# Performance work log

Measured on AMD Instinct MI355X. Metric: run time of the kernel, lower is better.

The kernel has to match this reference:

```python
import jax, jax.numpy as jnp
import numpy as np

NUM_AGENTS = 1000
N_ACTIONS = 16
HIDDEN = 256
COMM_STEPS = 4
B, M = 1024, 64


def setup_inputs() -> dict:
    key = jax.random.key(0)
    ks = jax.random.split(key, 8)
    agent_ids = jax.random.randint(ks[0], (B, M), 0, NUM_AGENTS)
    emb = jax.random.normal(ks[1], (NUM_AGENTS, HIDDEN), dtype=jnp.float32) * 0.1
    s1 = 1.0 / np.sqrt(3 * HIDDEN)
    W1 = jax.random.uniform(ks[2], (3 * HIDDEN, HIDDEN), jnp.float32, -s1, s1)
    b1 = jax.random.uniform(ks[3], (HIDDEN,), jnp.float32, -s1, s1)
    s2 = 1.0 / np.sqrt(HIDDEN)
    W2 = jax.random.uniform(ks[4], (HIDDEN, HIDDEN), jnp.float32, -s2, s2)
    b2 = jax.random.uniform(ks[5], (HIDDEN,), jnp.float32, -s2, s2)
    Wd = jax.random.uniform(ks[6], (HIDDEN, N_ACTIONS), jnp.float32, -s2, s2)
    bd = jax.random.uniform(ks[7], (N_ACTIONS,), jnp.float32, -s2, s2)
    return {"agent_ids": agent_ids, "emb": emb, "W1": W1, "b1": b1,
            "W2": W2, "b2": b2, "Wd": Wd, "bd": bd}


def reference(agent_ids, emb, W1, b1, W2, b2, Wd, bd):
    # h0: (B, M, H) embedding lookup
    h0 = emb[agent_ids]
    h = h0
    m = agent_ids.shape[1]
    inv = 1.0 / (m - 1)
    for _ in range(COMM_STEPS):
        # mean of other agents' hidden states: c_j = (sum_k h_k - h_j)/(M-1)
        c = (jnp.sum(h, axis=1, keepdims=True) - h) * inv
        x = jnp.concatenate([h, c, h0], axis=-1)  # (B, M, 3H)
        delta = jax.nn.relu(jnp.einsum('bmi,ih->bmh', x, W1) + b1)
        delta = jnp.einsum('bmi,ih->bmh', delta, W2) + b2
        h = h + delta  # residual (use_skip=True)
    logits = jnp.einsum('bmh,ha->bma', h, Wd) + bd
    return logits
```

## Files before the change

kernel.cpp:

```cpp
#include <hip/hip_runtime.h>

#define HID 256
#define NB 1024
#define NACT 16

typedef __bf16 bf16x8 __attribute__((ext_vector_type(8)));
typedef float  f32x4  __attribute__((ext_vector_type(4)));

#define HA_LO   32768
#define BUF0    65536
#define BUF1    98304
#define LDS_TOT 131072

#define PREP_N (4 * 65536 + 4096)

__device__ __forceinline__ void gload_lds16(const void* g, void* l) {
    __builtin_amdgcn_global_load_lds(
        (const __attribute__((address_space(1))) void*)g,
        (__attribute__((address_space(3))) void*)l, 16, 0, 0);
}
__device__ __forceinline__ unsigned short f2bf(float x) {
    union { float f; unsigned u; } v; v.f = x;
    unsigned r = v.u + 0x7fff + ((v.u >> 16) & 1);
    return (unsigned short)(r >> 16);
}
__device__ __forceinline__ float bf2f(unsigned short b) {
    union { float f; unsigned u; } v; v.u = ((unsigned)b) << 16;
    return v.f;
}
__device__ __forceinline__ float b2f_lo(unsigned v) { return bf2f((unsigned short)(v & 0xffffu)); }
__device__ __forceinline__ float b2f_hi(unsigned v) { return bf2f((unsigned short)(v >> 16)); }

__global__ __launch_bounds__(256) void prep_k(const float* __restrict__ W1,
                                              const float* __restrict__ W2,
                                              const float* __restrict__ Wd,
                                              unsigned short* __restrict__ WAh, unsigned short* __restrict__ WAl,
                                              unsigned short* __restrict__ WHh, unsigned short* __restrict__ WHl,
                                              unsigned short* __restrict__ WBh, unsigned short* __restrict__ WBl,
                                              unsigned short* __restrict__ WDh, unsigned short* __restrict__ WDl,
                                              float* __restrict__ Wc) {
    int i = blockIdx.x * 256 + threadIdx.x;
    const float inv = 1.0f / 63.0f;
    if (i < 65536) {
        int n = i >> 8, k = i & 255;
        float val = W1[k * 256 + n] - inv * W1[(256 + k) * 256 + n];
        unsigned short hi = f2bf(val);
        WAh[i] = hi; WAl[i] = f2bf(val - bf2f(hi));
    } else if (i < 2 * 65536) {
        int j = i - 65536, n = j >> 8, k = j & 255;
        float val = W1[(512 + k) * 256 + n];
        unsigned short hi = f2bf(val);
        WHh[j] = hi; WHl[j] = f2bf(val - bf2f(hi));
    } else if (i < 3 * 65536) {
        int j = i - 2 * 65536, n = j >> 8, k = j & 255;
        float val = W2[k * 256 + n];
        unsigned short hi = f2bf(val);
        WBh[j] = hi; WBl[j] = f2bf(val - bf2f(hi));
    } else if (i < 4 * 65536) {
        int j = i - 3 * 65536, k = j >> 8, n = j & 255;
        Wc[j] = inv * W1[(256 + k) * 256 + n];
    } else if (i < PREP_N) {
        int j = i - 4 * 65536, a = j >> 8, k = j & 255;
        float val = Wd[k * 16 + a];
        unsigned short hi = f2bf(val);
        WDh[j] = hi; WDl[j] = f2bf(val - bf2f(hi));
    }
}

__device__ __forceinline__ void kloopKar(const unsigned short* __restrict__ Wh,
                                         const unsigned short* __restrict__ Wl,
                                         char* lds, f32x4 (&acc)[2][4],
                                         int tid, int wm, int wn, int l15, int g)
{
    char* hA = lds;
    const int rxA = (l15 & 7) << 4;
    const int rowA0 = (wm * 32 + l15) * 512;
    const int rowA1 = rowA0 + 16 * 512;

    __syncthreads();
    #pragma unroll
    for (int p = 0; p < 2; ++p) {
        int c = p * 512 + tid;
        int n = c >> 2, s = c & 3;
        int sp = s ^ ((n >> 1) & 3);
        gload_lds16(Wh + (size_t)n * 256 + sp * 8, lds + BUF0 + c * 16);
        gload_lds16(Wl + (size_t)n * 256 + sp * 8, lds + BUF0 + 16384 + c * 16);
    }
    __syncthreads();

    #pragma unroll 2
    for (int kq = 0; kq < 8; ++kq) {
        const int cur = kq & 1;
        if (kq + 1 < 8) {
            const int kk = (kq + 1) * 32;
            char* dst = lds + (cur ? BUF0 : BUF1);
            #pragma unroll
            for (int p = 0; p < 2; ++p) {
                int c = p * 512 + tid;
                int n = c >> 2, s = c & 3;
                int sp = s ^ ((n >> 1) & 3);
                gload_lds16(Wh + (size_t)n * 256 + kk + sp * 8, dst + c * 16);
                gload_lds16(Wl + (size_t)n * 256 + kk + sp * 8, dst + 16384 + c * 16);
            }
        }
        const char* bb = lds + (cur ? BUF1 : BUF0);
        const int cb = (kq * 64 + g * 16) ^ rxA;
        bf16x8 a0h = *(const bf16x8*)(hA + rowA0 + cb);
        bf16x8 a1h = *(const bf16x8*)(hA + rowA1 + cb);
        bf16x8 a0l = *(const bf16x8*)(hA + HA_LO + rowA0 + cb);
        bf16x8 a1l = *(const bf16x8*)(hA + HA_LO + rowA1 + cb);
        #pragma unroll
        for (int nt = 0; nt < 4; ++nt) {
            int nn = wn * 64 + nt * 16 + l15;
            int off = nn * 64 + ((g ^ ((nn >> 1) & 3)) << 4);
            bf16x8 bh = *(const bf16x8*)(bb + off);
            bf16x8 bl = *(const bf16x8*)(bb + 16384 + off);
            acc[0][nt] = __builtin_amdgcn_mfma_f32_16x16x32_bf16(a0h, bh, acc[0][nt], 0, 0, 0);
            acc[1][nt] = __builtin_amdgcn_mfma_f32_16x16x32_bf16(a1h, bh, acc[1][nt], 0, 0, 0);
            acc[0][nt] = __builtin_amdgcn_mfma_f32_16x16x32_bf16(a0l, bh, acc[0][nt], 0, 0, 0);
            acc[1][nt] = __builtin_amdgcn_mfma_f32_16x16x32_bf16(a1l, bh, acc[1][nt], 0, 0, 0);
            acc[0][nt] = __builtin_amdgcn_mfma_f32_16x16x32_bf16(a0h, bl, acc[0][nt], 0, 0, 0);
            acc[1][nt] = __builtin_amdgcn_mfma_f32_16x16x32_bf16(a1h, bl, acc[1][nt], 0, 0, 0);
        }
        __syncthreads();
    }
}

__device__ __forceinline__ void STfun(char* lds, const float* __restrict__ Wc, int tid)
{
    char* hA = lds;
    float* Sp = (float*)(lds + BUF0);
    float* Sf = (float*)(lds + BUF0 + 4096);
    float* Tp = (float*)(lds + BUF0 + 8192);
    __syncthreads();
    {
        int ww = tid & 127, gq = tid >> 7;
        float s0 = 0.f, s1 = 0.f;
        #pragma unroll 4
        for (int m = gq * 16; m < gq * 16 + 16; ++m) {
            int byte = m * 512 + ((ww * 4) ^ ((m & 7) << 4));
            unsigned vh = *(const unsigned*)(hA + byte);
            unsigned vl = *(const unsigned*)(hA + HA_LO + byte);
            s0 += b2f_lo(vh) + b2f_lo(vl);
            s1 += b2f_hi(vh) + b2f_hi(vl);
        }
        Sp[gq * 256 + ww * 2] = s0;
        Sp[gq * 256 + ww * 2 + 1] = s1;
    }
    __syncthreads();
    if (tid < 256) Sf[tid] = (Sp[tid] + Sp[256 + tid]) + (Sp[512 + tid] + Sp[768 + tid]);
    __syncthreads();
    {
        int n = tid & 255, kh = tid >> 8;
        float a = 0.f;
        #pragma unroll 8
        for (int k = kh * 128; k < kh * 128 + 128; ++k)
            a += Sf[k] * Wc[(k << 8) + n];
        Tp[kh * 256 + n] = a;
    }
    __syncthreads();
}

__global__ __launch_bounds__(512, 2) void fused_all(
    const int* __restrict__ ids, const float* __restrict__ emb,
    const unsigned short* __restrict__ WAh, const unsigned short* __restrict__ WAl,
    const unsigned short* __restrict__ WHh, const unsigned short* __restrict__ WHl,
    const unsigned short* __restrict__ WBh, const unsigned short* __restrict__ WBl,
    const unsigned short* __restrict__ WDh, const unsigned short* __restrict__ WDl,
    const float* __restrict__ Wc,
    const float* __restrict__ b1, const float* __restrict__ b2,
    const float* __restrict__ bd, float* __restrict__ out)
{
    __shared__ __align__(16) char lds[LDS_TOT];
    const int tid = threadIdx.x;
    const int lane = tid & 63;
    const int w = tid >> 6;
    const int wm = w >> 2, wn = w & 3;
    const int l15 = lane & 15, g = lane >> 4;
    const size_t rowbase = (size_t)blockIdx.x * 64;
    char* hA = lds;
    float* Tp = (float*)(lds + BUF0 + 8192);

    {
        int r = tid >> 3, c0 = (tid & 7) * 32;
        int rx = (r & 7) << 4;
        const float4* src = (const float4*)(emb + (size_t)ids[rowbase + r] * HID + c0);
        char* dh = hA + r * 512;
        #pragma unroll
        for (int j = 0; j < 8; ++j) {
            float4 v = src[j];
            unsigned short h0 = f2bf(v.x), h1 = f2bf(v.y), h2 = f2bf(v.z), h3 = f2bf(v.w);
            unsigned short q0 = f2bf(v.x - bf2f(h0)), q1 = f2bf(v.y - bf2f(h1)),
                           q2 = f2bf(v.z - bf2f(h2)), q3 = f2bf(v.w - bf2f(h3));
            int byte = ((c0 + j * 4) * 2) ^ rx;
            *(uint2*)(dh + byte) = make_uint2((unsigned)h0 | ((unsigned)h1 << 16),
                                             (unsigned)h2 | ((unsigned)h3 << 16));
            *(uint2*)(dh + HA_LO + byte) = make_uint2((unsigned)q0 | ((unsigned)q1 << 16),
                                                      (unsigned)q2 | ((unsigned)q3 << 16));
        }
    }

    float b2r[4];
    #pragma unroll
    for (int nt = 0; nt < 4; ++nt) b2r[nt] = b2[wn * 64 + nt * 16 + l15];

    STfun(lds, Wc, tid);
    float tvr[4];
    #pragma unroll
    for (int nt = 0; nt < 4; ++nt) {
        int col = wn * 64 + nt * 16 + l15;
        tvr[nt] = Tp[col] + Tp[256 + col];
    }

    f32x4 acc[2][4], u0r[2][4];
    #pragma unroll
    for (int mt = 0; mt < 2; ++mt)
        #pragma unroll
        for (int nt = 0; nt < 4; ++nt) acc[mt][nt] = (f32x4){0.f, 0.f, 0.f, 0.f};

    for (int s = 0; s < 4; ++s) {
        if (s == 0) {
            kloopKar(WHh, WHl, lds, acc, tid, wm, wn, l15, g);
            #pragma unroll
            for (int nt = 0; nt < 4; ++nt) {
                float bb = b1[wn * 64 + nt * 16 + l15];
                #pragma unroll
                for (int mt = 0; mt < 2; ++mt)
                    #pragma unroll
                    for (int q = 0; q < 4; ++q) {
                        u0r[mt][nt][q] = acc[mt][nt][q] + bb;
                        acc[mt][nt][q] = 0.f;
                    }
            }
        }
        #pragma unroll
        for (int mt = 0; mt < 2; ++mt)
            #pragma unroll
            for (int nt = 0; nt < 4; ++nt)
                #pragma unroll
                for (int q = 0; q < 4; ++q)
                    acc[mt][nt][q] = tvr[nt] + u0r[mt][nt][q];
        kloopKar(WAh, WAl, lds, acc, tid, wm, wn, l15, g);

        #pragma unroll
        for (int mt = 0; mt < 2; ++mt)
            #pragma unroll
            for (int nt = 0; nt < 4; ++nt)
                #pragma unroll
                for (int q = 0; q < 4; ++q) {
                    int row = wm * 32 + mt * 16 + g * 4 + q;
                    int col = wn * 64 + nt * 16 + l15;
                    int byte = row * 512 + ((col * 2) ^ ((row & 7) << 4));
                    float hres = bf2f(*(const unsigned short*)(hA + byte))
                               + bf2f(*(const unsigned short*)(hA + HA_LO + byte));
                    float a = fmaxf(acc[mt][nt][q], 0.f);
                    unsigned short hi = f2bf(a);
                    *(unsigned short*)(hA + byte) = hi;
                    *(unsigned short*)(hA + HA_LO + byte) = f2bf(a - bf2f(hi));
                    acc[mt][nt][q] = hres + b2r[nt];
                }

        kloopKar(WBh, WBl, lds, acc, tid, wm, wn, l15, g);

        #pragma unroll
        for (int mt = 0; mt < 2; ++mt)
            #pragma unroll
            for (int nt = 0; nt < 4; ++nt)
                #pragma unroll
                for (int q = 0; q < 4; ++q) {
                    int row = wm * 32 + mt * 16 + g * 4 + q;
                    int col = wn * 64 + nt * 16 + l15;
                    int byte = row * 512 + ((col * 2) ^ ((row & 7) << 4));
                    float hv = acc[mt][nt][q];
                    unsigned short hi = f2bf(hv);
                    *(unsigned short*)(hA + byte) = hi;
                    *(unsigned short*)(hA + HA_LO + byte) = f2bf(hv - bf2f(hi));
                    acc[mt][nt][q] = 0.f;
                }

        if (s < 3) {
            STfun(lds, Wc, tid);
            #pragma unroll
            for (int nt = 0; nt < 4; ++nt) {
                int col = wn * 64 + nt * 16 + l15;
                tvr[nt] = Tp[col] + Tp[256 + col];
            }
        }
    }

    __syncthreads();
    {
        float* Dp = (float*)(lds + BUF0);
        f32x4 dacc[4];
        #pragma unroll
        for (int mi = 0; mi < 4; ++mi) dacc[mi] = (f32x4){0.f, 0.f, 0.f, 0.f};
        const int k = w * 32;
        bf16x8 wdh = *(const bf16x8*)(WDh + (size_t)l15 * 256 + k + g * 8);
        bf16x8 wdl = *(const bf16x8*)(WDl + (size_t)l15 * 256 + k + g * 8);
        #pragma unroll
        for (int mi = 0; mi < 4; ++mi) {
            int m = mi * 16 + l15;
            int byte = m * 512 + ((k * 2 + g * 16) ^ ((m & 7) << 4));
            bf16x8 hh = *(const bf16x8*)(hA + byte);
            bf16x8 hl = *(const bf16x8*)(hA + HA_LO + byte);
            dacc[mi] = __builtin_amdgcn_mfma_f32_16x16x32_bf16(wdh, hh, dacc[mi], 0, 0, 0);
            dacc[mi] = __builtin_amdgcn_mfma_f32_16x16x32_bf16(wdl, hh, dacc[mi], 0, 0, 0);
            dacc[mi] = __builtin_amdgcn_mfma_f32_16x16x32_bf16(wdh, hl, dacc[mi], 0, 0, 0);
        }
        #pragma unroll
        for (int mi = 0; mi < 4; ++mi)
            #pragma unroll
            for (int q = 0; q < 4; ++q)
                Dp[w * 1024 + (mi * 16 + l15) * 16 + g * 4 + q] = dacc[mi][q];
    }
    __syncthreads();
    {
        float* Dp = (float*)(lds + BUF0);
        int m = tid >> 3, a0 = (tid & 7) * 2;
        float o0 = bd[a0], o1 = bd[a0 + 1];
        #pragma unroll
        for (int w8 = 0; w8 < 8; ++w8) {
            o0 += Dp[w8 * 1024 + m * 16 + a0];
            o1 += Dp[w8 * 1024 + m * 16 + a0 + 1];
        }
        *(float2*)(out + ((size_t)rowbase + m) * NACT + a0) = make_float2(o0, o1);
    }
}

extern "C" void kernel_launch(void* const* d_in, const int* in_sizes, int n_in,
                              void* d_out, int out_size, void* d_ws, size_t ws_size,
                              hipStream_t stream) {
    const int*   ids = (const int*)d_in[0];
    const float* emb = (const float*)d_in[1];
    const float* W1  = (const float*)d_in[2];
    const float* b1  = (const float*)d_in[3];
    const float* W2  = (const float*)d_in[4];
    const float* b2  = (const float*)d_in[5];
    const float* Wd  = (const float*)d_in[6];
    const float* bd  = (const float*)d_in[7];
    float* out = (float*)d_out;

    char* p = (char*)d_ws;
    unsigned short* WAh = (unsigned short*)p; p += 65536 * 2;
    unsigned short* WAl = (unsigned short*)p; p += 65536 * 2;
    unsigned short* WHh = (unsigned short*)p; p += 65536 * 2;
    unsigned short* WHl = (unsigned short*)p; p += 65536 * 2;
    unsigned short* WBh = (unsigned short*)p; p += 65536 * 2;
    unsigned short* WBl = (unsigned short*)p; p += 65536 * 2;
    unsigned short* WDh = (unsigned short*)p; p += 4096 * 2;
    unsigned short* WDl = (unsigned short*)p; p += 4096 * 2;
    float* Wc = (float*)p;

    prep_k<<<(PREP_N + 255) / 256, 256, 0, stream>>>(W1, W2, Wd, WAh, WAl, WHh, WHl,
                                                     WBh, WBl, WDh, WDl, Wc);
    fused_all<<<NB, 512, 0, stream>>>(ids, emb, WAh, WAl, WHh, WHl, WBh, WBl,
                                      WDh, WDl, Wc, b1, b2, bd, out);
}
```

Measured before the change: 327.7 us.

## Stream weight fragments directly from global/L2 instead of staging through LDS

The prep kernel now writes the split bf16 weights pre-swizzled into MFMA fragment order. The GEMM loop loads B fragments directly from global memory (expected to hit L2) rather than double-buffering them into LDS. Each wave now covers all 64 rows by 32 columns instead of a 32x64 tile, and the per-k-step block barriers are gone. LDS use per block drops from 128KB to 80KB. In exchange, every wave loads its weights from L2 with nothing in between to hide the latency, and the final logits reduction uses only 4 waves.

```diff
diff --git a/kernel.cpp b/kernel.cpp
--- a/kernel.cpp
+++ b/kernel.cpp
@@ -8,17 +8,11 @@
 typedef float  f32x4  __attribute__((ext_vector_type(4)));
 
 #define HA_LO   32768
-#define BUF0    65536
-#define BUF1    98304
-#define LDS_TOT 131072
+#define OV      65536
+#define LDS_TOT 81920
 
 #define PREP_N (4 * 65536 + 4096)
 
-__device__ __forceinline__ void gload_lds16(const void* g, void* l) {
-    __builtin_amdgcn_global_load_lds(
-        (const __attribute__((address_space(1))) void*)g,
-        (__attribute__((address_space(3))) void*)l, 16, 0, 0);
-}
 __device__ __forceinline__ unsigned short f2bf(float x) {
     union { float f; unsigned u; } v; v.f = x;
     unsigned r = v.u + 0x7fff + ((v.u >> 16) & 1);
@@ -41,21 +35,22 @@
                                               float* __restrict__ Wc) {
     int i = blockIdx.x * 256 + threadIdx.x;
     const float inv = 1.0f / 63.0f;
-    if (i < 65536) {
-        int n = i >> 8, k = i & 255;
-        float val = W1[k * 256 + n] - inv * W1[(256 + k) * 256 + n];
+    if (i < 3 * 65536) {
+        int mat = i >> 16, j = i & 65535;
+        int kq = j >> 13, r = j & 8191;
+        int nb = r >> 9, r2 = r & 511;
+        int l = r2 >> 3, e = r2 & 7;
+        int n = nb * 16 + (l & 15);
+        int k = kq * 32 + (l >> 4) * 8 + e;
+        float val;
+        if (mat == 0)      val = W1[k * 256 + n] - inv * W1[(256 + k) * 256 + n];
+        else if (mat == 1) val = W1[(512 + k) * 256 + n];
+        else               val = W2[k * 256 + n];
         unsigned short hi = f2bf(val);
-        WAh[i] = hi; WAl[i] = f2bf(val - bf2f(hi));
-    } else if (i < 2 * 65536) {
-        int j = i - 65536, n = j >> 8, k = j & 255;
-        float val = W1[(512 + k) * 256 + n];
-        unsigned short hi = f2bf(val);
-        WHh[j] = hi; WHl[j] = f2bf(val - bf2f(hi));
-    } else if (i < 3 * 65536) {
-        int j = i - 2 * 65536, n = j >> 8, k = j & 255;
-        float val = W2[k * 256 + n];
-        unsigned short hi = f2bf(val);
-        WBh[j] = hi; WBl[j] = f2bf(val - bf2f(hi));
+        unsigned short lo = f2bf(val - bf2f(hi));
+        if (mat == 0)      { WAh[j] = hi; WAl[j] = lo; }
+        else if (mat == 1) { WHh[j] = hi; WHl[j] = lo; }
+        else               { WBh[j] = hi; WBl[j] = lo; }
     } else if (i < 4 * 65536) {
         int j = i - 3 * 65536, k = j >> 8, n = j & 255;
         Wc[j] = inv * W1[(256 + k) * 256 + n];
@@ -67,71 +62,44 @@
     }
 }
 
-__device__ __forceinline__ void kloopKar(const unsigned short* __restrict__ Wh,
-                                         const unsigned short* __restrict__ Wl,
-                                         char* lds, f32x4 (&acc)[2][4],
-                                         int tid, int wm, int wn, int l15, int g)
+__device__ __forceinline__ void kloopL2(const unsigned short* __restrict__ Wfh,
+                                        const unsigned short* __restrict__ Wfl,
+                                        const char* hA, f32x4 (&acc)[4][2],
+                                        int w, int lane, int l15, int g)
 {
-    char* hA = lds;
     const int rxA = (l15 & 7) << 4;
-    const int rowA0 = (wm * 32 + l15) * 512;
-    const int rowA1 = rowA0 + 16 * 512;
-
-    __syncthreads();
-    #pragma unroll
-    for (int p = 0; p < 2; ++p) {
-        int c = p * 512 + tid;
-        int n = c >> 2, s = c & 3;
-        int sp = s ^ ((n >> 1) & 3);
-        gload_lds16(Wh + (size_t)n * 256 + sp * 8, lds + BUF0 + c * 16);
-        gload_lds16(Wl + (size_t)n * 256 + sp * 8, lds + BUF0 + 16384 + c * 16);
-    }
-    __syncthreads();
-
+    const size_t lbase = ((size_t)(w * 2) * 64 + lane) * 8;
     #pragma unroll 2
     for (int kq = 0; kq < 8; ++kq) {
-        const int cur = kq & 1;
-        if (kq + 1 < 8) {
-            const int kk = (kq + 1) * 32;
-            char* dst = lds + (cur ? BUF0 : BUF1);
-            #pragma unroll
-            for (int p = 0; p < 2; ++p) {
-                int c = p * 512 + tid;
-                int n = c >> 2, s = c & 3;
-                int sp = s ^ ((n >> 1) & 3);
-                gload_lds16(Wh + (size_t)n * 256 + kk + sp * 8, dst + c * 16);
-                gload_lds16(Wl + (size_t)n * 256 + kk + sp * 8, dst + 16384 + c * 16);
+        const int cb = (kq * 64 + g * 16) ^ rxA;
+        bf16x8 ah[4], al[4];
+        #pragma unroll
+        for (int mt = 0; mt < 4; ++mt) {
+            int rb = (mt * 16 + l15) * 512;
+            ah[mt] = *(const bf16x8*)(hA + rb + cb);
+            al[mt] = *(const bf16x8*)(hA + HA_LO + rb + cb);
+        }
+        const size_t kb = (size_t)kq * 8192 + lbase;
+        #pragma unroll
+        for (int nt = 0; nt < 2; ++nt) {
+            bf16x8 bh = *(const bf16x8*)(Wfh + kb + nt * 512);
+            bf16x8 bl = *(const bf16x8*)(Wfl + kb + nt * 512);
+            #pragma unroll
+            for (int mt = 0; mt < 4; ++mt) {
+                acc[mt][nt] = __builtin_amdgcn_mfma_f32_16x16x32_bf16(ah[mt], bh, acc[mt][nt], 0, 0, 0);
+                acc[mt][nt] = __builtin_amdgcn_mfma_f32_16x16x32_bf16(al[mt], bh, acc[mt][nt], 0, 0, 0);
+                acc[mt][nt] = __builtin_amdgcn_mfma_f32_16x16x32_bf16(ah[mt], bl, acc[mt][nt], 0, 0, 0);
             }
         }
-        const char* bb = lds + (cur ? BUF1 : BUF0);
-        const int cb = (kq * 64 + g * 16) ^ rxA;
-        bf16x8 a0h = *(const bf16x8*)(hA + rowA0 + cb);
-        bf16x8 a1h = *(const bf16x8*)(hA + rowA1 + cb);
-        bf16x8 a0l = *(const bf16x8*)(hA + HA_LO + rowA0 + cb);
-        bf16x8 a1l = *(const bf16x8*)(hA + HA_LO + rowA1 + cb);
-        #pragma unroll
-        for (int nt = 0; nt < 4; ++nt) {
-            int nn = wn * 64 + nt * 16 + l15;
-            int off = nn * 64 + ((g ^ ((nn >> 1) & 3)) << 4);
-            bf16x8 bh = *(const bf16x8*)(bb + off);
-            bf16x8 bl = *(const bf16x8*)(bb + 16384 + off);
-            acc[0][nt] = __builtin_amdgcn_mfma_f32_16x16x32_bf16(a0h, bh, acc[0][nt], 0, 0, 0);
-            acc[1][nt] = __builtin_amdgcn_mfma_f32_16x16x32_bf16(a1h, bh, acc[1][nt], 0, 0, 0);
-            acc[0][nt] = __builtin_amdgcn_mfma_f32_16x16x32_bf16(a0l, bh, acc[0][nt], 0, 0, 0);
-            acc[1][nt] = __builtin_amdgcn_mfma_f32_16x16x32_bf16(a1l, bh, acc[1][nt], 0, 0, 0);
-            acc[0][nt] = __builtin_amdgcn_mfma_f32_16x16x32_bf16(a0h, bl, acc[0][nt], 0, 0, 0);
-            acc[1][nt] = __builtin_amdgcn_mfma_f32_16x16x32_bf16(a1h, bl, acc[1][nt], 0, 0, 0);
-        }
-        __syncthreads();
     }
 }
 
 __device__ __forceinline__ void STfun(char* lds, const float* __restrict__ Wc, int tid)
 {
     char* hA = lds;
-    float* Sp = (float*)(lds + BUF0);
-    float* Sf = (float*)(lds + BUF0 + 4096);
-    float* Tp = (float*)(lds + BUF0 + 8192);
+    float* Sp = (float*)(lds + OV);
+    float* Sf = (float*)(lds + OV + 4096);
+    float* Tp = (float*)(lds + OV + 8192);
     __syncthreads();
     {
         int ww = tid & 127, gq = tid >> 7;
@@ -175,11 +143,10 @@
     const int tid = threadIdx.x;
     const int lane = tid & 63;
     const int w = tid >> 6;
-    const int wm = w >> 2, wn = w & 3;
     const int l15 = lane & 15, g = lane >> 4;
     const size_t rowbase = (size_t)blockIdx.x * 64;
     char* hA = lds;
-    float* Tp = (float*)(lds + BUF0 + 8192);
+    float* Tp = (float*)(lds + OV + 8192);
 
     {
         int r = tid >> 3, c0 = (tid & 7) * 32;
@@ -200,32 +167,28 @@
         }
     }
 
-    float b2r[4];
+    STfun(lds, Wc, tid);
+    float tvr[2];
     #pragma unroll
-    for (int nt = 0; nt < 4; ++nt) b2r[nt] = b2[wn * 64 + nt * 16 + l15];
-
-    STfun(lds, Wc, tid);
-    float tvr[4];
+    for (int nt = 0; nt < 2; ++nt) {
+        int col = w * 32 + nt * 16 + l15;
+        tvr[nt] = Tp[col] + Tp[256 + col];
+    }
+
+    f32x4 acc[4][2], u0r[4][2];
     #pragma unroll
-    for (int nt = 0; nt < 4; ++nt) {
-        int col = wn * 64 + nt * 16 + l15;
-        tvr[nt] = Tp[col] + Tp[256 + col];
-    }
-
-    f32x4 acc[2][4], u0r[2][4];
-    #pragma unroll
-    for (int mt = 0; mt < 2; ++mt)
-        #pragma unroll
-        for (int nt = 0; nt < 4; ++nt) acc[mt][nt] = (f32x4){0.f, 0.f, 0.f, 0.f};
+    for (int mt = 0; mt < 4; ++mt)
+        #pragma unroll
+        for (int nt = 0; nt < 2; ++nt) acc[mt][nt] = (f32x4){0.f, 0.f, 0.f, 0.f};
 
     for (int s = 0; s < 4; ++s) {
         if (s == 0) {
-            kloopKar(WHh, WHl, lds, acc, tid, wm, wn, l15, g);
-            #pragma unroll
-            for (int nt = 0; nt < 4; ++nt) {
-                float bb = b1[wn * 64 + nt * 16 + l15];
-                #pragma unroll
-                for (int mt = 0; mt < 2; ++mt)
+            kloopL2(WHh, WHl, hA, acc, w, lane, l15, g);
+            #pragma unroll
+            for (int nt = 0; nt < 2; ++nt) {
+                float bb = b1[w * 32 + nt * 16 + l15];
+                #pragma unroll
+                for (int mt = 0; mt < 4; ++mt)
                     #pragma unroll
                     for (int q = 0; q < 4; ++q) {
                         u0r[mt][nt][q] = acc[mt][nt][q] + bb;
@@ -234,42 +197,48 @@
             }
         }
         #pragma unroll
-        for (int mt = 0; mt < 2; ++mt)
-            #pragma unroll
-            for (int nt = 0; nt < 4; ++nt)
+        for (int mt = 0; mt < 4; ++mt)
+            #pragma unroll
+            for (int nt = 0; nt < 2; ++nt)
                 #pragma unroll
                 for (int q = 0; q < 4; ++q)
                     acc[mt][nt][q] = tvr[nt] + u0r[mt][nt][q];
-        kloopKar(WAh, WAl, lds, acc, tid, wm, wn, l15, g);
-
-        #pragma unroll
-        for (int mt = 0; mt < 2; ++mt)
-            #pragma unroll
-            for (int nt = 0; nt < 4; ++nt)
+        kloopL2(WAh, WAl, hA, acc, w, lane, l15, g);
+
+        __syncthreads();
+        {
+            float b2r0 = b2[w * 32 + l15], b2r1 = b2[w * 32 + 16 + l15];
+            #pragma unroll
+            for (int mt = 0; mt < 4; ++mt)
+                #pragma unroll
+                for (int nt = 0; nt < 2; ++nt)
+                    #pragma unroll
+                    for (int q = 0; q < 4; ++q) {
+                        int row = mt * 16 + g * 4 + q;
+                        int col = w * 32 + nt * 16 + l15;
+                        int byte = row * 512 + ((col * 2) ^ ((row & 7) << 4));
+                        float hres = bf2f(*(const unsigned short*)(hA + byte))
+                                   + bf2f(*(const unsigned short*)(hA + HA_LO + byte));
+                        float a = fmaxf(acc[mt][nt][q], 0.f);
+                        unsigned short hi = f2bf(a);
+                        *(unsigned short*)(hA + byte) = hi;
+                        *(unsigned short*)(hA + HA_LO + byte) = f2bf(a - bf2f(hi));
+                        acc[mt][nt][q] = hres + (nt ? b2r1 : b2r0);
+                    }
+        }
+        __syncthreads();
+
+        kloopL2(WBh, WBl, hA, acc, w, lane, l15, g);
+
+        __syncthreads();
+        #pragma unroll
+        for (int mt = 0; mt < 4; ++mt)
+            #pragma unroll
+            for (int nt = 0; nt < 2; ++nt)
                 #pragma unroll
                 for (int q = 0; q < 4; ++q) {
-                    int row = wm * 32 + mt * 16 + g * 4 + q;
-                    int col = wn * 64 + nt * 16 + l15;
-                    int byte = row * 512 + ((col * 2) ^ ((row & 7) << 4));
-                    float hres = bf2f(*(const unsigned short*)(hA + byte))
-                               + bf2f(*(const unsigned short*)(hA + HA_LO + byte));
-                    float a = fmaxf(acc[mt][nt][q], 0.f);
-                    unsigned short hi = f2bf(a);
-                    *(unsigned short*)(hA + byte) = hi;
-                    *(unsigned short*)(hA + HA_LO + byte) = f2bf(a - bf2f(hi));
-                    acc[mt][nt][q] = hres + b2r[nt];
-                }
-
-        kloopKar(WBh, WBl, lds, acc, tid, wm, wn, l15, g);
-
-        #pragma unroll
-        for (int mt = 0; mt < 2; ++mt)
-            #pragma unroll
-            for (int nt = 0; nt < 4; ++nt)
-                #pragma unroll
-                for (int q = 0; q < 4; ++q) {
-                    int row = wm * 32 + mt * 16 + g * 4 + q;
-                    int col = wn * 64 + nt * 16 + l15;
+                    int row = mt * 16 + g * 4 + q;
+                    int col = w * 32 + nt * 16 + l15;
                     int byte = row * 512 + ((col * 2) ^ ((row & 7) << 4));
                     float hv = acc[mt][nt][q];
                     unsigned short hi = f2bf(hv);
@@ -281,8 +250,8 @@
         if (s < 3) {
             STfun(lds, Wc, tid);
             #pragma unroll
-            for (int nt = 0; nt < 4; ++nt) {
-                int col = wn * 64 + nt * 16 + l15;
+            for (int nt = 0; nt < 2; ++nt) {
+                int col = w * 32 + nt * 16 + l15;
                 tvr[nt] = Tp[col] + Tp[256 + col];
             }
         }
@@ -290,38 +259,43 @@
 
     __syncthreads();
     {
-        float* Dp = (float*)(lds + BUF0);
-        f32x4 dacc[4];
-        #pragma unroll
-        for (int mi = 0; mi < 4; ++mi) dacc[mi] = (f32x4){0.f, 0.f, 0.f, 0.f};
-        const int k = w * 32;
-        bf16x8 wdh = *(const bf16x8*)(WDh + (size_t)l15 * 256 + k + g * 8);
-        bf16x8 wdl = *(const bf16x8*)(WDl + (size_t)l15 * 256 + k + g * 8);
-        #pragma unroll
-        for (int mi = 0; mi < 4; ++mi) {
-            int m = mi * 16 + l15;
-            int byte = m * 512 + ((k * 2 + g * 16) ^ ((m & 7) << 4));
-            bf16x8 hh = *(const bf16x8*)(hA + byte);
-            bf16x8 hl = *(const bf16x8*)(hA + HA_LO + byte);
-            dacc[mi] = __builtin_amdgcn_mfma_f32_16x16x32_bf16(wdh, hh, dacc[mi], 0, 0, 0);
-            dacc[mi] = __builtin_amdgcn_mfma_f32_16x16x32_bf16(wdl, hh, dacc[mi], 0, 0, 0);
-            dacc[mi] = __builtin_amdgcn_mfma_f32_16x16x32_bf16(wdh, hl, dacc[mi], 0, 0, 0);
-        }
-        #pragma unroll
-        for (int mi = 0; mi < 4; ++mi)
-            #pragma unroll
-            for (int q = 0; q < 4; ++q)
-                Dp[w * 1024 + (mi * 16 + l15) * 16 + g * 4 + q] = dacc[mi][q];
-    }
-    __syncthreads();
-    {
-        float* Dp = (float*)(lds + BUF0);
+        float* Dp = (float*)(lds + OV);
+        if (w < 4) {
+            f32x4 dacc[4];
+            #pragma unroll
+            for (int mi = 0; mi < 4; ++mi) dacc[mi] = (f32x4){0.f, 0.f, 0.f, 0.f};
+            #pragma unroll
+            for (int kh = 0; kh < 2; ++kh) {
+                const int k = w * 64 + kh * 32;
+                bf16x8 wdh = *(const bf16x8*)(WDh + (size_t)l15 * 256 + k + g * 8);
+                bf16x8 wdl = *(const bf16x8*)(WDl + (size_t)l15 * 256 + k + g * 8);
+                #pragma unroll
+                for (int mi = 0; mi < 4; ++mi) {
+                    int m = mi * 16 + l15;
+                    int byte = m * 512 + ((k * 2 + g * 16) ^ ((m & 7) << 4));
+                    bf16x8 hh = *(const bf16x8*)(hA + byte);
+                    bf16x8 hl = *(const bf16x8*)(hA + HA_LO + byte);
+                    dacc[mi] = __builtin_amdgcn_mfma_f32_16x16x32_bf16(wdh, hh, dacc[mi], 0, 0, 0);
+                    dacc[mi] = __builtin_amdgcn_mfma_f32_16x16x32_bf16(wdl, hh, dacc[mi], 0, 0, 0);
+                    dacc[mi] = __builtin_amdgcn_mfma_f32_16x16x32_bf16(wdh, hl, dacc[mi], 0, 0, 0);
+                }
+            }
+            #pragma unroll
+            for (int mi = 0; mi < 4; ++mi)
+                #pragma unroll
+                for (int q = 0; q < 4; ++q)
+                    Dp[w * 1024 + (mi * 16 + l15) * 16 + g * 4 + q] = dacc[mi][q];
+        }
+    }
+    __syncthreads();
+    {
+        float* Dp = (float*)(lds + OV);
         int m = tid >> 3, a0 = (tid & 7) * 2;
         float o0 = bd[a0], o1 = bd[a0 + 1];
         #pragma unroll
-        for (int w8 = 0; w8 < 8; ++w8) {
-            o0 += Dp[w8 * 1024 + m * 16 + a0];
-            o1 += Dp[w8 * 1024 + m * 16 + a0 + 1];
+        for (int w4 = 0; w4 < 4; ++w4) {
+            o0 += Dp[w4 * 1024 + m * 16 + a0];
+            o1 += Dp[w4 * 1024 + m * 16 + a0 + 1];
         }
         *(float2*)(out + ((size_t)rowbase + m) * NACT + a0) = make_float2(o0, o1);
     }
```

After: 273.4 us. -16.6%, faster.
